# Optimization experiments

Measured on AMD Instinct MI355X. Metric: run time of the kernel, lower is better.

## Reference

```python
import jax, jax.numpy as jnp
import numpy as np

D_MODEL = 256
NHEAD = 8
HEAD_DIM = D_MODEL // NHEAD
EPS = 1e-6
LN_EPS = 1e-5


def embed_rotary(x, cos, sin):
    # x, cos, sin: [N, L, C]; rotate even/odd pairs (Lepard-style RoFPE)
    x2 = jnp.stack([-x[..., 1::2], x[..., ::2]], axis=-1).reshape(x.shape)
    return x * cos + x2 * sin


def layer_norm(x, g, b):
    m = jnp.mean(x, axis=-1, keepdims=True)
    v = jnp.mean((x - m) ** 2, axis=-1, keepdims=True)
    return (x - m) / jnp.sqrt(v + LN_EPS) * g + b


def setup_inputs() -> dict:
    key = jax.random.key(0)
    ks = jax.random.split(key, 12)
    N, L, S, C = 8, 4096, 4096, D_MODEL
    s = 1.0 / np.sqrt(C)
    return {
        "x": jax.random.normal(ks[0], (N, L, C), jnp.float32),
        "source": jax.random.normal(ks[1], (N, S, C), jnp.float32),
        "x_pe": jax.random.normal(ks[2], (N, L, C, 2), jnp.float32),
        "source_pe": jax.random.normal(ks[3], (N, S, C, 2), jnp.float32),
        "Wq": jax.random.normal(ks[4], (C, C), jnp.float32) * s,
        "Wk": jax.random.normal(ks[5], (C, C), jnp.float32) * s,
        "Wv": jax.random.normal(ks[6], (C, C), jnp.float32) * s,
        "Wm": jax.random.normal(ks[7], (C, C), jnp.float32) * s,
        "W1": jax.random.normal(ks[8], (2 * C, 2 * C), jnp.float32) * s,
        "W2": jax.random.normal(ks[9], (2 * C, C), jnp.float32) * s,
        "ln1_g": jnp.ones((C,), jnp.float32),
        "ln1_b": jnp.zeros((C,), jnp.float32),
        "ln2_g": jnp.ones((C,), jnp.float32),
        "ln2_b": jnp.zeros((C,), jnp.float32),
    }


def reference(x, source, x_pe, source_pe, Wq, Wk, Wv, Wm, W1, W2, ln1_g, ln1_b, ln2_g, ln2_b):
    N, L, C = x.shape
    S = source.shape[1]
    H, D = NHEAD, HEAD_DIM

    query = x @ Wq           # [N, L, C]
    key = source @ Wk        # [N, S, C]
    value = source @ Wv      # [N, S, C]

    # ELU+1 feature maps (on pre-rotary projections)
    Q = jax.nn.elu(query) + 1.0
    K = jax.nn.elu(key) + 1.0

    q_cos, q_sin = x_pe[..., 0], x_pe[..., 1]
    k_cos, k_sin = source_pe[..., 0], source_pe[..., 1]
    Q_pos = embed_rotary(query, q_cos, q_sin)
    K_pos = embed_rotary(key, k_cos, k_sin)
    value = embed_rotary(value, k_cos, k_sin)

    Q = Q.reshape(N, L, H, D)
    K = K.reshape(N, S, H, D)
    Q_pos = Q_pos.reshape(N, L, H, D)
    K_pos = K_pos.reshape(N, S, H, D)
    value = value.reshape(N, S, H, D)

    values = value / S
    KV = jnp.einsum('nshd,nshv->nhdv', K_pos, values)          # [N, H, D, D]
    Z = 1.0 / (jnp.einsum('nlhd,nhd->nlh', Q, K.sum(axis=1)) + EPS)
    queried = jnp.einsum('nlhd,nhdv->nlhv', Q_pos, KV) * Z[..., None] * S  # [N, L, H, D]

    message = queried.reshape(N, L, C) @ Wm
    message = layer_norm(message, ln1_g, ln1_b)
    h = jnp.concatenate([x, message], axis=2) @ W1             # [N, L, 2C]
    h = jax.nn.relu(h)
    message = h @ W2                                            # [N, L, C]
    message = layer_norm(message, ln2_g, ln2_b)
    return x + message
```

## Files before the change

### kernel.cpp

```cpp
#include <hip/hip_runtime.h>

typedef __attribute__((ext_vector_type(8))) short bf16x8;
typedef __attribute__((ext_vector_type(4))) float f32x4;

__device__ __forceinline__ float bf2f(unsigned short b) {
    unsigned u = ((unsigned)b) << 16; float f;
    __builtin_memcpy(&f, &u, 4); return f;
}
__device__ __forceinline__ unsigned short f2bf(float f) {
    unsigned u; __builtin_memcpy(&u, &f, 4);
    unsigned r = u + 0x7FFFu + ((u >> 16) & 1u);
    return (unsigned short)(r >> 16);
}
__device__ __forceinline__ unsigned packbf(float a, float b) {
    return (unsigned)f2bf(a) | ((unsigned)f2bf(b) << 16);
}
__device__ __forceinline__ float elu1(float v) { return v > 0.f ? v + 1.f : __expf(v); }

__device__ __forceinline__ void async_copy16(const unsigned short* g, unsigned short* l) {
    __builtin_amdgcn_global_load_lds(
        (const __attribute__((address_space(1))) unsigned int*)g,
        (__attribute__((address_space(3))) unsigned int*)l, 16, 0, 0);
}

__device__ __host__ __forceinline__ int chan_of(int tc) {
    return (tc & ~63) | ((tc & 15) << 1) | ((tc >> 4) & 1) | (((tc >> 5) & 1) << 5);
}
__device__ __forceinline__ int chan_even(int gnb, int p, int low) {
    const int tc = gnb + 32 * p + low;
    return (tc & ~63) | ((tc & 15) << 1) | (((tc >> 5) & 1) << 5);
}

#define EPI_RELU 0
#define EPI_Q 1
#define EPI_KV 2
#define EPI_LN1 3
#define EPI_LN2RES 4

template <int MT, int NT, int EPI>
__global__ __launch_bounds__(256, 4) void gemm_bt(
    const unsigned short* __restrict__ A, int lda,
    const unsigned short* __restrict__ B, int K,
    unsigned short* __restrict__ Cb, int ldc,
    const float* __restrict__ pe,
    const float* __restrict__ KsumC, float* __restrict__ KsumA,
    float* __restrict__ Zbuf, unsigned short* __restrict__ Qpos,
    unsigned short* __restrict__ KF, unsigned short* __restrict__ VF,
    const float* __restrict__ g, const float* __restrict__ bta,
    unsigned short* __restrict__ A2out,
    const float* __restrict__ xres, float* __restrict__ outF)
{
    constexpr int WM = MT / 2, WN = NT / 2, MI = WM / 16, NI = WN / 16;
    __shared__ unsigned short Asm[2][MT * 32];
    __shared__ unsigned short Bsm[2][NT * 32];
    const int t = threadIdx.x;
    const int lane = t & 63, w = t >> 6;
    const int wm = w & 1, wn = w >> 1;
    const int quad = lane >> 4, low = lane & 15;
    const int m0 = blockIdx.x * MT, n0 = blockIdx.y * NT;

    f32x4 acc[MI][NI];
#pragma unroll
    for (int i = 0; i < MI; i++)
#pragma unroll
        for (int j = 0; j < NI; j++) acc[i][j] = (f32x4){0.f, 0.f, 0.f, 0.f};

    auto stage = [&](int k0, int buf) {
#pragma unroll
        for (int i = 0; i < MT / 64; i++) {
            const int chunk = i * 256 + t;
            const int row = chunk >> 2;
            const int part = (chunk & 3) ^ ((chunk >> 3) & 3);
            async_copy16(A + (size_t)(m0 + row) * lda + k0 + part * 8,
                         &Asm[buf][(i * 256 + w * 64) * 8]);
        }
#pragma unroll
        for (int i = 0; i < NT / 64; i++) {
            const int chunk = i * 256 + t;
            const int row = chunk >> 2;
            const int part = (chunk & 3) ^ ((chunk >> 3) & 3);
            async_copy16(B + (size_t)(n0 + row) * K + k0 + part * 8,
                         &Bsm[buf][(i * 256 + w * 64) * 8]);
        }
    };

    const int nk = K >> 5;
    const int swz = (low >> 1) & 3;
    stage(0, 0);
    int kb = 0;
    for (int ks = 0; ks < nk; ks++, kb ^= 1) {
        asm volatile("s_waitcnt vmcnt(0)" ::: "memory");
        __builtin_amdgcn_s_barrier();
        __builtin_amdgcn_sched_barrier(0);
        if (ks + 1 < nk) stage((ks + 1) << 5, kb ^ 1);
        bf16x8 a[MI], b[NI];
#pragma unroll
        for (int mi = 0; mi < MI; mi++)
            a[mi] = *(const bf16x8*)&Asm[kb][(wm * WM + mi * 16 + low) * 32 + ((quad ^ swz)) * 8];
#pragma unroll
        for (int ni = 0; ni < NI; ni++)
            b[ni] = *(const bf16x8*)&Bsm[kb][(wn * WN + ni * 16 + low) * 32 + ((quad ^ swz)) * 8];
#pragma unroll
        for (int mi = 0; mi < MI; mi++)
#pragma unroll
            for (int ni = 0; ni < NI; ni++)
                acc[mi][ni] = __builtin_amdgcn_mfma_f32_16x16x32_bf16(a[mi], b[ni], acc[mi][ni], 0, 0, 0);
    }

    const int gmb = m0 + wm * WM, gnb = n0 + wn * WN;

    if constexpr (EPI == EPI_RELU) {
#pragma unroll
        for (int mi = 0; mi < MI; mi++)
#pragma unroll
            for (int p = 0; p < NI / 2; p++) {
                const int c_e = chan_even(gnb, p, low);
#pragma unroll
                for (int r = 0; r < 4; r++) {
                    const int row = gmb + mi * 16 + quad * 4 + r;
                    const float ve = acc[mi][2 * p][r], vo = acc[mi][2 * p + 1][r];
                    *(unsigned*)&Cb[(size_t)row * ldc + c_e] =
                        packbf(ve > 0.f ? ve : 0.f, vo > 0.f ? vo : 0.f);
                }
            }
    } else if constexpr (EPI == EPI_Q) {
        const int n = m0 >> 12;
#pragma unroll
        for (int p = 0; p < NI / 2; p++) {
            const int c_e = chan_even(gnb, p, low);
            const int head = c_e >> 5;
            const float2 ks = *(const float2*)&KsumC[n * 256 + c_e];
#pragma unroll
            for (int mi = 0; mi < MI; mi++) {
#pragma unroll
                for (int r = 0; r < 4; r++) {
                    const int row = gmb + mi * 16 + quad * 4 + r;
                    const float4 cs = *(const float4*)&pe[((size_t)row * 256 + c_e) * 2];
                    const float ve = acc[mi][2 * p][r], vo = acc[mi][2 * p + 1][r];
                    *(unsigned*)&Qpos[(size_t)row * 256 + c_e] =
                        packbf(ve * cs.x - vo * cs.y, vo * cs.z + ve * cs.w);
                    float z = elu1(ve) * ks.x + elu1(vo) * ks.y;
                    z += __shfl_xor(z, 1); z += __shfl_xor(z, 2);
                    z += __shfl_xor(z, 4); z += __shfl_xor(z, 8);
                    if (low == 0) Zbuf[(size_t)row * 8 + head] = 1.f / (z + 1e-6f);
                }
            }
        }
    } else if constexpr (EPI == EPI_KV) {
        const int n = m0 >> 12;
#pragma unroll
        for (int p = 0; p < NI / 2; p++) {
            const int tcg = gnb + 32 * p;
            const bool isK = ((tcg >> 5) & 1) == 0;
            const int c = ((tcg & ~63) >> 1) | (low << 1);
            const int nh = n * 8 + (c >> 5), d = c & 31;
            unsigned short* dst = isK ? KF : VF;
            float kel_e = 0.f, kel_o = 0.f;
#pragma unroll
            for (int mi = 0; mi < MI; mi++) {
                const int row0 = gmb + mi * 16 + quad * 4;
                const int s0 = row0 & 4095;
                unsigned short pk[8];
#pragma unroll
                for (int r = 0; r < 4; r++) {
                    const int row = row0 + r;
                    const float4 cs = *(const float4*)&pe[((size_t)row * 256 + c) * 2];
                    const float ve = acc[mi][2 * p][r], vo = acc[mi][2 * p + 1][r];
                    pk[r]     = f2bf(ve * cs.x - vo * cs.y);
                    pk[4 + r] = f2bf(vo * cs.z + ve * cs.w);
                    if (isK) { kel_e += elu1(ve); kel_o += elu1(vo); }
                }
                const size_t base = ((size_t)nh * 512 + (s0 >> 3)) * 32;
                *(uint2*)&dst[(base + d) * 8 + (s0 & 7)]     = *(const uint2*)&pk[0];
                *(uint2*)&dst[(base + d + 1) * 8 + (s0 & 7)] = *(const uint2*)&pk[4];
            }
            if (isK) {
                kel_e += __shfl_xor(kel_e, 16); kel_e += __shfl_xor(kel_e, 32);
                kel_o += __shfl_xor(kel_o, 16); kel_o += __shfl_xor(kel_o, 32);
                if (quad == 0) {
                    atomicAdd(&KsumA[n * 256 + c], kel_e);
                    atomicAdd(&KsumA[n * 256 + c + 1], kel_o);
                }
            }
        }
    } else {
        __shared__ float2 lnp[2][64];
        __syncthreads();
#pragma unroll
        for (int mi = 0; mi < MI; mi++)
#pragma unroll
            for (int r = 0; r < 4; r++) {
                float s1 = 0.f, s2 = 0.f;
#pragma unroll
                for (int ni = 0; ni < NI; ni++) {
                    const float v = acc[mi][ni][r];
                    s1 += v; s2 += v * v;
                }
                s1 += __shfl_xor(s1, 1); s2 += __shfl_xor(s2, 1);
                s1 += __shfl_xor(s1, 2); s2 += __shfl_xor(s2, 2);
                s1 += __shfl_xor(s1, 4); s2 += __shfl_xor(s2, 4);
                s1 += __shfl_xor(s1, 8); s2 += __shfl_xor(s2, 8);
                if (low == 0) lnp[wn][wm * WM + mi * 16 + quad * 4 + r] = make_float2(s1, s2);
            }
        __syncthreads();
#pragma unroll
        for (int mi = 0; mi < MI; mi++)
#pragma unroll
            for (int r = 0; r < 4; r++) {
                const int rl = wm * WM + mi * 16 + quad * 4 + r;
                const int row = m0 + rl;
                const float2 pa = lnp[0][rl], pb = lnp[1][rl];
                const float mean = (pa.x + pb.x) * (1.f / 256.f);
                const float var = (pa.y + pb.y) * (1.f / 256.f) - mean * mean;
                const float rstd = rsqrtf(var + 1e-5f);
#pragma unroll
                for (int p = 0; p < NI / 2; p++) {
                    const int c_e = chan_even(gnb, p, low);
                    const float2 gg = *(const float2*)&g[c_e];
                    const float2 bb = *(const float2*)&bta[c_e];
                    const float ve = acc[mi][2 * p][r], vo = acc[mi][2 * p + 1][r];
                    const float oe = (ve - mean) * rstd * gg.x + bb.x;
                    const float oo = (vo - mean) * rstd * gg.y + bb.y;
                    if constexpr (EPI == EPI_LN1) {
                        *(unsigned*)&A2out[(size_t)row * 512 + 256 + c_e] = packbf(oe, oo);
                    } else {
                        const float2 xv = *(const float2*)&xres[(size_t)row * 256 + c_e];
                        float2 o; o.x = xv.x + oe; o.y = xv.y + oo;
                        *(float2*)&outF[(size_t)row * 256 + c_e] = o;
                    }
                }
            }
    }
}

__global__ void prep_weights(const float* __restrict__ Wq, const float* __restrict__ Wk,
                             const float* __restrict__ Wv, const float* __restrict__ Wm,
                             const float* __restrict__ W1, const float* __restrict__ W2,
                             unsigned short* __restrict__ WqT, unsigned short* __restrict__ WkvT,
                             unsigned short* __restrict__ WmT, unsigned short* __restrict__ W1T,
                             unsigned short* __restrict__ W2T, float* __restrict__ zero_base) {
    const int idx = blockIdx.x * 256 + threadIdx.x;
    if (idx < 65536) {
        const int tc = idx >> 8, k = idx & 255;
        WqT[idx] = f2bf(Wq[(size_t)k * 256 + chan_of(tc)]);
    } else if (idx < 196608) {
        const int i = idx - 65536, tc = i >> 8, k = i & 255;
        const int f = (tc >> 5) & 1;
        const int c = ((tc & ~63) >> 1) | ((tc & 15) << 1) | ((tc >> 4) & 1);
        WkvT[i] = f2bf(f ? Wv[(size_t)k * 256 + c] : Wk[(size_t)k * 256 + c]);
    } else if (idx < 262144) {
        const int i = idx - 196608, tc = i >> 8, k = i & 255;
        WmT[i] = f2bf(Wm[(size_t)k * 256 + chan_of(tc)]);
    } else if (idx < 524288) {
        const int i = idx - 262144, tc = i >> 9, k = i & 511;
        W1T[i] = f2bf(W1[(size_t)k * 512 + chan_of(tc)]);
    } else if (idx < 655360) {
        const int i = idx - 524288, tc = i >> 9, k = i & 511;
        W2T[i] = f2bf(W2[(size_t)k * 256 + chan_of(tc)]);
    } else {
        zero_base[idx - 655360] = 0.f;
    }
}

__global__ void conv_bf16(const float* __restrict__ src, unsigned short* __restrict__ dst, int dstride) {
    const int idx = blockIdx.x * 256 + threadIdx.x;
    const int row = idx >> 6;
    const int c0 = (idx & 63) * 4;
    const float4 v = *(const float4*)&src[(size_t)row * 256 + c0];
    unsigned short o[4] = {f2bf(v.x), f2bf(v.y), f2bf(v.z), f2bf(v.w)};
    *(uint2*)&dst[(size_t)row * dstride + c0] = *(const uint2*)o;
}

__global__ __launch_bounds__(256) void kv2_kernel(const unsigned short* __restrict__ KF,
                                                  const unsigned short* __restrict__ VF,
                                                  float* __restrict__ KVT) {
    const int nh = blockIdx.x, sc = blockIdx.y;
    const int t = threadIdx.x, lane = t & 63, w = t >> 6;
    const int quad = lane >> 4, low = lane & 15;
    const int sbase = sc * 1024 + w * 256;

    f32x4 acc[2][2];
#pragma unroll
    for (int i = 0; i < 2; i++)
#pragma unroll
        for (int j = 0; j < 2; j++) acc[i][j] = (f32x4){0.f, 0.f, 0.f, 0.f};

    for (int s0 = 0; s0 < 256; s0 += 32) {
        const int sk = sbase + s0 + quad * 8;
        const size_t cb = ((size_t)nh * 512 + (sk >> 3)) * 32;
        bf16x8 a[2], b[2];
#pragma unroll
        for (int mi = 0; mi < 2; mi++)
            a[mi] = *(const bf16x8*)&KF[(cb + mi * 16 + low) * 8];
#pragma unroll
        for (int ni = 0; ni < 2; ni++)
            b[ni] = *(const bf16x8*)&VF[(cb + ni * 16 + low) * 8];
#pragma unroll
        for (int mi = 0; mi < 2; mi++)
#pragma unroll
            for (int ni = 0; ni < 2; ni++)
                acc[mi][ni] = __builtin_amdgcn_mfma_f32_16x16x32_bf16(a[mi], b[ni], acc[mi][ni], 0, 0, 0);
    }

    __shared__ float red[4][1024];
#pragma unroll
    for (int mi = 0; mi < 2; mi++)
#pragma unroll
        for (int ni = 0; ni < 2; ni++)
#pragma unroll
            for (int r = 0; r < 4; r++)
                red[w][(mi * 16 + quad * 4 + r) * 32 + ni * 16 + low] = acc[mi][ni][r];
    __syncthreads();
#pragma unroll
    for (int k = 0; k < 4; k++) {
        const int i = t + k * 256;
        const float s = red[0][i] + red[1][i] + red[2][i] + red[3][i];
        atomicAdd(&KVT[(size_t)nh * 1024 + (size_t)(i & 31) * 32 + (i >> 5)], s);
    }
}

__global__ __launch_bounds__(256) void attn_out_kernel(const unsigned short* __restrict__ Qpos,
                                                       const float* __restrict__ KVT,
                                                       const float* __restrict__ Zbuf,
                                                       unsigned short* __restrict__ Qrd) {
    const int h = blockIdx.y, mt = blockIdx.x;
    const int t = threadIdx.x, lane = t & 63, w = t >> 6;
    const int quad = lane >> 4, low = lane & 15;
    const int rbase = mt * 256 + w * 64;
    const int n = rbase >> 12;

    bf16x8 b[2];
#pragma unroll
    for (int ni = 0; ni < 2; ni++) {
        const float* src = &KVT[((size_t)(n * 8 + h) * 32 + ni * 16 + low) * 32 + quad * 8];
        short tmp[8];
#pragma unroll
        for (int j = 0; j < 8; j++) tmp[j] = (short)f2bf(src[j]);
        __builtin_memcpy(&b[ni], tmp, 16);
    }

    f32x4 acc[4][2];
#pragma unroll
    for (int i = 0; i < 4; i++)
#pragma unroll
        for (int j = 0; j < 2; j++) acc[i][j] = (f32x4){0.f, 0.f, 0.f, 0.f};

#pragma unroll
    for (int mi = 0; mi < 4; mi++) {
        const bf16x8 a = *(const bf16x8*)&Qpos[((size_t)(rbase + mi * 16 + low)) * 256 + h * 32 + quad * 8];
#pragma unroll
        for (int ni = 0; ni < 2; ni++)
            acc[mi][ni] = __builtin_amdgcn_mfma_f32_16x16x32_bf16(a, b[ni], acc[mi][ni], 0, 0, 0);
    }

#pragma unroll
    for (int mi = 0; mi < 4; mi++)
#pragma unroll
        for (int ni = 0; ni < 2; ni++)
#pragma unroll
            for (int r = 0; r < 4; r++) {
                const int row = rbase + mi * 16 + quad * 4 + r;
                const int col = h * 32 + ni * 16 + low;
                Qrd[(size_t)row * 256 + col] = f2bf(acc[mi][ni][r] * Zbuf[(size_t)row * 8 + h]);
            }
}

extern "C" void kernel_launch(void* const* d_in, const int* in_sizes, int n_in,
                              void* d_out, int out_size, void* d_ws, size_t ws_size,
                              hipStream_t stream) {
    const float* x   = (const float*)d_in[0];
    const float* src = (const float*)d_in[1];
    const float* xpe = (const float*)d_in[2];
    const float* spe = (const float*)d_in[3];
    const float* Wq  = (const float*)d_in[4];
    const float* Wk  = (const float*)d_in[5];
    const float* Wv  = (const float*)d_in[6];
    const float* Wm  = (const float*)d_in[7];
    const float* W1  = (const float*)d_in[8];
    const float* W2  = (const float*)d_in[9];
    const float* g1  = (const float*)d_in[10];
    const float* b1  = (const float*)d_in[11];
    const float* g2  = (const float*)d_in[12];
    const float* b2  = (const float*)d_in[13];

    char* p = (char*)d_ws;
    unsigned short* WqT  = (unsigned short*)p; p += 256 * 256 * 2;
    unsigned short* WkvT = (unsigned short*)p; p += 512 * 256 * 2;
    unsigned short* WmT  = (unsigned short*)p; p += 256 * 256 * 2;
    unsigned short* W1T  = (unsigned short*)p; p += 512 * 512 * 2;
    unsigned short* W2T  = (unsigned short*)p; p += 256 * 512 * 2;
    float* KVT  = (float*)p; p += 64 * 1024 * 4;
    float* Ksum = (float*)p; p += 8 * 256 * 4;
    float* Zbuf = (float*)p; p += (size_t)32768 * 8 * 4;
    unsigned short* A2   = (unsigned short*)p; p += (size_t)32768 * 512 * 2;
    unsigned short* srcB = (unsigned short*)p; p += (size_t)32768 * 256 * 2;
    unsigned short* KF   = (unsigned short*)p; p += (size_t)32768 * 256 * 2;
    unsigned short* VF   = (unsigned short*)p; p += (size_t)32768 * 256 * 2;
    unsigned short* Qpos = (unsigned short*)p; p += (size_t)32768 * 256 * 2;
    unsigned short* Qrd  = (unsigned short*)p; p += (size_t)32768 * 256 * 2;
    unsigned short* hbuf = KF;

    prep_weights<<<2824, 256, 0, stream>>>(Wq, Wk, Wv, Wm, W1, W2,
                                           WqT, WkvT, WmT, W1T, W2T, KVT);
    conv_bf16<<<8192, 256, 0, stream>>>(x, A2, 512);
    conv_bf16<<<8192, 256, 0, stream>>>(src, srcB, 256);

    gemm_bt<64, 256, EPI_KV><<<dim3(512, 2), 256, 0, stream>>>(
        srcB, 256, WkvT, 256, nullptr, 0, spe, nullptr, Ksum,
        nullptr, nullptr, KF, VF, nullptr, nullptr, nullptr, nullptr, nullptr);
    kv2_kernel<<<dim3(64, 4), 256, 0, stream>>>(KF, VF, KVT);

    gemm_bt<64, 256, EPI_Q><<<dim3(512, 1), 256, 0, stream>>>(
        A2, 512, WqT, 256, nullptr, 0, xpe, Ksum, nullptr,
        Zbuf, Qpos, nullptr, nullptr, nullptr, nullptr, nullptr, nullptr, nullptr);

    attn_out_kernel<<<dim3(128, 8), 256, 0, stream>>>(Qpos, KVT, Zbuf, Qrd);

    gemm_bt<64, 256, EPI_LN1><<<512, 256, 0, stream>>>(
        Qrd, 256, WmT, 256, nullptr, 0, nullptr, nullptr, nullptr,
        nullptr, nullptr, nullptr, nullptr, g1, b1, A2, nullptr, nullptr);

    gemm_bt<64, 256, EPI_RELU><<<dim3(512, 2), 256, 0, stream>>>(
        A2, 512, W1T, 512, hbuf, 512, nullptr, nullptr, nullptr,
        nullptr, nullptr, nullptr, nullptr, nullptr, nullptr, nullptr, nullptr, nullptr);

    gemm_bt<64, 256, EPI_LN2RES><<<512, 256, 0, stream>>>(
        hbuf, 512, W2T, 512, nullptr, 0, nullptr, nullptr, nullptr,
        nullptr, nullptr, nullptr, nullptr, g2, b2, nullptr, x, (float*)d_out);
}
```

Baseline: 391.9 us.

## Triple-buffer GEMM LDS staging with partial vmcnt waits and narrower N tiles

Moves the GEMM main loop from double to triple buffering. Loads for step k+2 are issued while step k computes, and the wait is only until the older batch of async copies has landed (vmcnt 3 or 5). The launch-bounds occupancy hint is dropped, and the KV, Q and ReLU GEMMs switch from 256-wide to 128-wide N tiles, doubling their grids. This raises LDS use per block and may lower occupancy. The extra __syncthreads before the LN epilogue is removed, which relies on the epilogue not reusing the staging buffers.

```diff
diff --git a/kernel.cpp b/kernel.cpp
--- a/kernel.cpp
+++ b/kernel.cpp
@@ -38,7 +38,7 @@
 #define EPI_LN2RES 4
 
 template <int MT, int NT, int EPI>
-__global__ __launch_bounds__(256, 4) void gemm_bt(
+__global__ __launch_bounds__(256) void gemm_bt(
     const unsigned short* __restrict__ A, int lda,
     const unsigned short* __restrict__ B, int K,
     unsigned short* __restrict__ Cb, int ldc,
@@ -51,8 +51,10 @@
     const float* __restrict__ xres, float* __restrict__ outF)
 {
     constexpr int WM = MT / 2, WN = NT / 2, MI = WM / 16, NI = WN / 16;
-    __shared__ unsigned short Asm[2][MT * 32];
-    __shared__ unsigned short Bsm[2][NT * 32];
+    constexpr int LPS = 1 + NT / 64;
+    static_assert(MT == 64, "A staging assumes MT*4 == 256 chunks");
+    __shared__ unsigned short Asm[3][MT * 32];
+    __shared__ unsigned short Bsm[3][NT * 32];
     const int t = threadIdx.x;
     const int lane = t & 63, w = t >> 6;
     const int wm = w & 1, wn = w >> 1;
@@ -66,13 +68,11 @@
         for (int j = 0; j < NI; j++) acc[i][j] = (f32x4){0.f, 0.f, 0.f, 0.f};
 
     auto stage = [&](int k0, int buf) {
-#pragma unroll
-        for (int i = 0; i < MT / 64; i++) {
-            const int chunk = i * 256 + t;
-            const int row = chunk >> 2;
-            const int part = (chunk & 3) ^ ((chunk >> 3) & 3);
+        {
+            const int row = t >> 2;
+            const int part = (t & 3) ^ ((t >> 3) & 3);
             async_copy16(A + (size_t)(m0 + row) * lda + k0 + part * 8,
-                         &Asm[buf][(i * 256 + w * 64) * 8]);
+                         &Asm[buf][(w * 64) * 8]);
         }
 #pragma unroll
         for (int i = 0; i < NT / 64; i++) {
@@ -87,12 +87,21 @@
     const int nk = K >> 5;
     const int swz = (low >> 1) & 3;
     stage(0, 0);
-    int kb = 0;
-    for (int ks = 0; ks < nk; ks++, kb ^= 1) {
-        asm volatile("s_waitcnt vmcnt(0)" ::: "memory");
+    stage(32, 1);
+    int kb = 0, sb = 2;
+    for (int ks = 0; ks < nk; ks++) {
+        __builtin_amdgcn_sched_barrier(0);
+        if (ks + 1 < nk) {
+            if constexpr (LPS == 3)
+                asm volatile("s_waitcnt vmcnt(3)" ::: "memory");
+            else
+                asm volatile("s_waitcnt vmcnt(5)" ::: "memory");
+        } else {
+            asm volatile("s_waitcnt vmcnt(0)" ::: "memory");
+        }
         __builtin_amdgcn_s_barrier();
         __builtin_amdgcn_sched_barrier(0);
-        if (ks + 1 < nk) stage((ks + 1) << 5, kb ^ 1);
+        if (ks + 2 < nk) stage((ks + 2) << 5, sb);
         bf16x8 a[MI], b[NI];
 #pragma unroll
         for (int mi = 0; mi < MI; mi++)
@@ -105,6 +114,8 @@
 #pragma unroll
             for (int ni = 0; ni < NI; ni++)
                 acc[mi][ni] = __builtin_amdgcn_mfma_f32_16x16x32_bf16(a[mi], b[ni], acc[mi][ni], 0, 0, 0);
+        kb = (kb == 2) ? 0 : kb + 1;
+        sb = (sb == 2) ? 0 : sb + 1;
     }
 
     const int gmb = m0 + wm * WM, gnb = n0 + wn * WN;
@@ -185,7 +196,6 @@
         }
     } else {
         __shared__ float2 lnp[2][64];
-        __syncthreads();
 #pragma unroll
         for (int mi = 0; mi < MI; mi++)
 #pragma unroll
@@ -405,12 +415,12 @@
     conv_bf16<<<8192, 256, 0, stream>>>(x, A2, 512);
     conv_bf16<<<8192, 256, 0, stream>>>(src, srcB, 256);
 
-    gemm_bt<64, 256, EPI_KV><<<dim3(512, 2), 256, 0, stream>>>(
+    gemm_bt<64, 128, EPI_KV><<<dim3(512, 4), 256, 0, stream>>>(
         srcB, 256, WkvT, 256, nullptr, 0, spe, nullptr, Ksum,
         nullptr, nullptr, KF, VF, nullptr, nullptr, nullptr, nullptr, nullptr);
     kv2_kernel<<<dim3(64, 4), 256, 0, stream>>>(KF, VF, KVT);
 
-    gemm_bt<64, 256, EPI_Q><<<dim3(512, 1), 256, 0, stream>>>(
+    gemm_bt<64, 128, EPI_Q><<<dim3(512, 2), 256, 0, stream>>>(
         A2, 512, WqT, 256, nullptr, 0, xpe, Ksum, nullptr,
         Zbuf, Qpos, nullptr, nullptr, nullptr, nullptr, nullptr, nullptr, nullptr);
 
@@ -420,7 +430,7 @@
         Qrd, 256, WmT, 256, nullptr, 0, nullptr, nullptr, nullptr,
         nullptr, nullptr, nullptr, nullptr, g1, b1, A2, nullptr, nullptr);
 
-    gemm_bt<64, 256, EPI_RELU><<<dim3(512, 2), 256, 0, stream>>>(
+    gemm_bt<64, 128, EPI_RELU><<<dim3(512, 4), 256, 0, stream>>>(
         A2, 512, W1T, 512, hbuf, 512, nullptr, nullptr, nullptr,
         nullptr, nullptr, nullptr, nullptr, nullptr, nullptr, nullptr, nullptr, nullptr);
 
```

Result: faster. 380.7 us (-2.9%).
